# Optimization experiments

Hardware: AMD Instinct MI355X
Metric: run time of the kernel (lower is better)

Reference implementation:

```python
import jax, jax.numpy as jnp
import numpy as np

B, IMG, D, HEADS, L, PC, PF, OUT = 8, 128, 128, 4, 2, 8, 4, 32
HC = IMG // PC; NC = HC * HC          # 16x16 -> 256 coarse tokens
HF = IMG // PF; NF = HF * HF          # 32x32 -> 1024 fine tokens


def _ln(x, g, b):
    m = x.mean(-1, keepdims=True)
    v = x.var(-1, keepdims=True)
    return (x - m) * jax.lax.rsqrt(v + 1e-5) * g + b


def _conv(x, w, b, pad):
    y = jax.lax.conv_general_dilated(x, w, (1, 1), ((pad, pad), (pad, pad)),
                                     dimension_numbers=('NCHW', 'OIHW', 'NCHW'))
    return y + b[None, :, None, None]


def _bilinear_ac(x, oh, ow):  # F.interpolate(mode='bilinear', align_corners=True)
    _, _, H, W = x.shape
    ys = jnp.linspace(0.0, H - 1.0, oh)
    xs = jnp.linspace(0.0, W - 1.0, ow)
    y0 = jnp.floor(ys).astype(jnp.int32); y1 = jnp.minimum(y0 + 1, H - 1); wy = (ys - y0)[:, None]
    x0 = jnp.floor(xs).astype(jnp.int32); x1 = jnp.minimum(x0 + 1, W - 1); wx = (xs - x0)[None, :]
    g = lambda yi, xi: x[:, :, yi][:, :, :, xi]
    return (g(y0, x0) * (1 - wy) * (1 - wx) + g(y0, x1) * (1 - wy) * wx
            + g(y1, x0) * wy * (1 - wx) + g(y1, x1) * wy * wx)


def _patchify(x, p):  # F.unfold with kernel=stride=p, in_chans=1
    b, _, h, w = x.shape
    return x.reshape(b, h // p, p, w // p, p).transpose(0, 1, 3, 2, 4).reshape(b, (h // p) * (w // p), p * p)


def _forward(x, Wpc, bpc, Wpf, bpf, type_embed, ln1_g, ln1_b, Wqkv, Wo, bo,
             ln2_g, ln2_b, W1, b1, W2, b2, dWc, dbc, dWf, dbf, fW1, fb1, fW2, fb2):
    Bx = x.shape[0]
    # ---- multi-scale patch embed ----
    coarse = _patchify(x, PC) @ Wpc + bpc + type_embed[0]   # [B,NC,D]
    fine = _patchify(x, PF) @ Wpf + bpf                     # [B,NF,D]
    # ---- edge map: sobel -> avgpool(4) -> threshold at per-image mean ----
    gray = x.mean(1, keepdims=True)
    kx = jnp.array([[[[-1, 0, 1], [-2, 0, 2], [-1, 0, 1]]]], x.dtype)
    ky = jnp.array([[[[-1, -2, -1], [0, 0, 0], [1, 2, 1]]]], x.dtype)
    sx = _conv(gray, kx, jnp.zeros((1,), x.dtype), 1)
    sy = _conv(gray, ky, jnp.zeros((1,), x.dtype), 1)
    e = jnp.sqrt(sx ** 2 + sy ** 2)
    e = e.reshape(Bx, 1, IMG // 4, 4, IMG // 4, 4).mean((3, 5))  # [B,1,32,32] == fine grid
    mask_flat = (e > e.mean((2, 3), keepdims=True)).reshape(Bx, NF)
    # ---- static-shape analogue of per-sample masked gather + pad_sequence:
    # stable sort puts edge tokens first (original pixel order preserved), pads are zeros
    order = jnp.argsort(jnp.logical_not(mask_flat), axis=1, stable=True)   # [B,NF]
    mask_sorted = jnp.take_along_axis(mask_flat, order, 1)
    fine_sorted = jnp.take_along_axis(fine, order[..., None], 1) * mask_sorted[..., None]
    fine_sorted = fine_sorted + type_embed[1]   # type embed added to pads too (as in torch)
    tokens = jnp.concatenate([coarse, fine_sorted], axis=1)   # [B,N,D]
    N = NC + NF
    hd = D // HEADS
    scale = hd ** -0.5
    # ---- encoder blocks (pre-LN attn + MLP, irregular-token path) ----
    for l in range(L):
        y = _ln(tokens, ln1_g[l], ln1_b[l])
        qkv = (y @ Wqkv[l]).reshape(Bx, N, 3, HEADS, hd).transpose(2, 0, 3, 1, 4)
        q, k, v = qkv[0], qkv[1], qkv[2]
        attn = jax.nn.softmax(jnp.einsum('bhqd,bhkd->bhqk', q, k) * scale, axis=-1)
        o = jnp.einsum('bhqk,bhkd->bhqd', attn, v).transpose(0, 2, 1, 3).reshape(Bx, N, D)
        tokens = tokens + o @ Wo[l] + bo[l]
        y = _ln(tokens, ln2_g[l], ln2_b[l])
        tokens = tokens + jax.nn.gelu(y @ W1[l] + b1[l], approximate=False) @ W2[l] + b2[l]
    # ---- multi-scale decoder ----
    c = (tokens[:, :NC] @ dWc + dbc).reshape(Bx, HC, HC, 1).transpose(0, 3, 1, 2)
    c_up = _bilinear_ac(c, OUT, OUT)
    feats = (tokens[:, NC:] @ dWf + dbf) * mask_sorted[..., None]   # pads stay zero
    inv = jnp.argsort(order, axis=1)                                # scatter back to pixel order
    f_flat = jnp.take_along_axis(feats, inv[..., None], 1)          # [B,NF,1]
    f_map = f_flat.reshape(Bx, HF, HF, 1).transpose(0, 3, 1, 2)
    f_up = _bilinear_ac(f_map, OUT, OUT)
    fused = jnp.concatenate([c_up, f_up], axis=1)
    h = jax.nn.relu(_conv(fused, fW1, fb1, 1))
    return _conv(h, fW2, fb2, 1)   # [B,1,32,32]


def setup_inputs() -> dict:
    key = jax.random.key(0)
    ks = jax.random.split(key, 16)
    n = lambda k, shape: jax.random.normal(k, shape, jnp.float32) * 0.02
    z = lambda *shape: jnp.zeros(shape, jnp.float32)
    return {
        'x': jax.random.normal(ks[0], (B, 1, IMG, IMG), jnp.float32),
        'Wpc': n(ks[1], (PC * PC, D)), 'bpc': z(D),
        'Wpf': n(ks[2], (PF * PF, D)), 'bpf': z(D),
        'type_embed': n(ks[3], (2, D)),
        'ln1_g': jnp.ones((L, D), jnp.float32), 'ln1_b': z(L, D),
        'Wqkv': n(ks[4], (L, D, 3 * D)),
        'Wo': n(ks[5], (L, D, D)), 'bo': z(L, D),
        'ln2_g': jnp.ones((L, D), jnp.float32), 'ln2_b': z(L, D),
        'W1': n(ks[6], (L, D, 2 * D)), 'b1': z(L, 2 * D),
        'W2': n(ks[7], (L, 2 * D, D)), 'b2': z(L, D),
        'dWc': n(ks[8], (D, 1)), 'dbc': z(1),
        'dWf': n(ks[9], (D, 1)), 'dbf': z(1),
        'fW1': n(ks[10], (2, 2, 3, 3)) * 10.0, 'fb1': z(2),
        'fW2': n(ks[11], (1, 2, 3, 3)) * 10.0, 'fb2': z(1),
    }


def reference(x, Wpc, bpc, Wpf, bpf, type_embed, ln1_g, ln1_b, Wqkv, Wo, bo,
              ln2_g, ln2_b, W1, b1, W2, b2, dWc, dbc, dWf, dbf, fW1, fb1, fW2, fb2):
    return _forward(x, Wpc, bpc, Wpf, bpf, type_embed, ln1_g, ln1_b, Wqkv, Wo, bo,
                    ln2_g, ln2_b, W1, b1, W2, b2, dWc, dbc, dWf, dbf, fW1, fb1, fW2, fb2)
```

## Files before the change

### kernel.cpp

```cpp
#include <hip/hip_runtime.h>
#include <math.h>

#define Bx 8
#define IMG 128
#define DD 128
#define HEADS 4
#define LL 2
#define PCc 8
#define PFf 4
#define HCc 16
#define NCc 256
#define HFf 32
#define NFf 1024
#define NTOK 1280
#define HD 32
#define SPLIT 4
#define NQT 20

typedef __attribute__((ext_vector_type(8))) short short8;
typedef __attribute__((ext_vector_type(4))) float f32x4;

__device__ __forceinline__ short f2bf(float f) {
  unsigned u = __builtin_bit_cast(unsigned, f);
  u += 0x7FFF + ((u >> 16) & 1);
  return (short)(u >> 16);
}
__device__ __forceinline__ float bf2f(short s) {
  unsigned u = ((unsigned)(unsigned short)s) << 16;
  return __builtin_bit_cast(float, u);
}

__global__ __launch_bounds__(256) void k_prologue(const float* __restrict__ x,
    const float* __restrict__ Wpc, const float* __restrict__ bpc,
    const float* __restrict__ Wpf, const float* __restrict__ bpf,
    const float* __restrict__ te,
    const float* __restrict__ Wqkv, const float* __restrict__ Wo,
    const float* __restrict__ W1, const float* __restrict__ W2,
    short* __restrict__ WtQKV, short* __restrict__ WtO,
    short* __restrict__ Wt1, short* __restrict__ Wt2,
    float* __restrict__ e, float* __restrict__ tokens,
    float* __restrict__ fineb) {
  int blk = blockIdx.x;
  int t = threadIdx.x;
  if (blk < 1024) {
    int idx = blk * 256 + t;
    int l = idx / 131072, r = idx % 131072;
    const float* src; short* dst; int N, off;
    if (r < 49152)      { src = Wqkv + l * 49152; dst = WtQKV + l * 49152; N = 384; off = r; }
    else if (r < 65536) { src = Wo + l * 16384;  dst = WtO + l * 16384;  N = 128; off = r - 49152; }
    else if (r < 98304) { src = W1 + l * 32768;  dst = Wt1 + l * 32768;  N = 256; off = r - 65536; }
    else                { src = W2 + l * 32768;  dst = Wt2 + l * 32768;  N = 128; off = r - 98304; }
    int k = off / N, n = off % N;
    int K = (r >= 98304) ? 256 : 128;
    dst[(size_t)n * K + k] = f2bf(src[off]);
  } else if (blk < 1536) {
    int bt = blk - 1024;
    int b = bt >> 6, tile = bt & 63;
    int ty = tile >> 3, tx = tile & 7;
    int ly = t >> 4, lx = t & 15;
    int py = ty * 16 + ly, px = tx * 16 + lx;
    const float* img = x + (size_t)b * IMG * IMG;
    float v[3][3];
    #pragma unroll
    for (int ky = 0; ky < 3; ++ky)
      #pragma unroll
      for (int kx = 0; kx < 3; ++kx) {
        int yy = py + ky - 1, xx = px + kx - 1;
        v[ky][kx] = (yy >= 0 && yy < IMG && xx >= 0 && xx < IMG)
                        ? img[yy * IMG + xx] : 0.f;
      }
    float gx = -v[0][0] + v[0][2] - 2.f * v[1][0] + 2.f * v[1][2] - v[2][0] + v[2][2];
    float gy = -v[0][0] - 2.f * v[0][1] - v[0][2] + v[2][0] + 2.f * v[2][1] + v[2][2];
    __shared__ float sm[256];
    sm[t] = sqrtf(gx * gx + gy * gy);
    __syncthreads();
    if (t < 16) {
      int cy = t >> 2, cx = t & 3;
      float s = 0.f;
      #pragma unroll
      for (int dy = 0; dy < 4; ++dy)
        #pragma unroll
        for (int dx = 0; dx < 4; ++dx) s += sm[(cy * 4 + dy) * 16 + cx * 4 + dx];
      e[b * NFf + (ty * 4 + cy) * 32 + tx * 4 + cx] = s * (1.f / 16.f);
    }
  } else if (blk < 2560) {
    int bt = (blk - 1536) * 2 + (t >> 7);
    int b = bt / NCc, tok = bt % NCc;
    int hc = tok / HCc, wc = tok % HCc;
    int half = t >> 7, d = t & 127;
    __shared__ float patch[2][PCc * PCc];
    if (d < PCc * PCc) {
      int pi = d / PCc, pj = d % PCc;
      patch[half][d] = x[(b * IMG + hc * PCc + pi) * IMG + wc * PCc + pj];
    }
    __syncthreads();
    float acc = bpc[d] + te[d];
    #pragma unroll 8
    for (int i = 0; i < PCc * PCc; ++i) acc += patch[half][i] * Wpc[i * DD + d];
    tokens[(size_t)(b * NTOK + tok) * DD + d] = acc;
  } else {
    int ft = (blk - 2560) * 2 + (t >> 7);
    int b = ft >> 10, tloc = ft & 1023;
    int hf = tloc >> 5, wf = tloc & 31;
    int half = t >> 7, d = t & 127;
    __shared__ float patch[2][PFf * PFf];
    if (d < PFf * PFf) {
      int pi = d / PFf, pj = d % PFf;
      patch[half][d] = x[(b * IMG + hf * PFf + pi) * IMG + wf * PFf + pj];
    }
    __syncthreads();
    float acc = bpf[d];
    #pragma unroll
    for (int i = 0; i < PFf * PFf; ++i) acc += patch[half][i] * Wpf[i * DD + d];
    fineb[(size_t)(b * NFf + tloc) * DD + d] = acc;
  }
}

__global__ __launch_bounds__(1024) void k_edge_sort(const float* __restrict__ e,
    int* __restrict__ order, float* __restrict__ msort) {
  int b = blockIdx.x;
  int t = threadIdx.x;
  int lane = t & 63, wave = t >> 6;
  float ev = e[b * NFf + t];
  __shared__ float wsum[16];
  __shared__ int wcnt[16];
  float r = ev;
  #pragma unroll
  for (int o = 32; o > 0; o >>= 1) r += __shfl_xor(r, o, 64);
  if (lane == 0) wsum[wave] = r;
  __syncthreads();
  float tot = 0.f;
  #pragma unroll
  for (int i = 0; i < 16; ++i) tot += wsum[i];
  float mean = tot * (1.f / 1024.f);
  int m = (ev > mean) ? 1 : 0;
  unsigned long long bal = __ballot(m);
  if (lane == 0) wcnt[wave] = __popcll(bal);
  __syncthreads();
  int wbase = 0, total = 0;
  #pragma unroll
  for (int i = 0; i < 16; ++i) {
    int c = wcnt[i];
    if (i < wave) wbase += c;
    total += c;
  }
  unsigned long long below = (lane == 63) ? ~0ULL : ((1ULL << (lane + 1)) - 1);
  int incl = __popcll(bal & below);
  int eb = wbase + incl - m;
  int pos = m ? eb : (total + t - eb);
  order[b * NFf + pos] = t;
  msort[b * NFf + pos] = (float)m;
}

__global__ __launch_bounds__(256) void k_gather_ln(float* __restrict__ tokens,
    const float* __restrict__ fineb, const int* __restrict__ order,
    const float* __restrict__ msort, const float* __restrict__ te,
    const float* __restrict__ g, const float* __restrict__ bb,
    short* __restrict__ outp) {
  int row = blockIdx.x * 4 + (threadIdx.x >> 6);
  int lane = threadIdx.x & 63;
  int b = row / NTOK, r = row % NTOK;
  float2 v;
  if (r < NCc) {
    v = ((const float2*)(tokens + (size_t)row * DD))[lane];
  } else {
    int pos = r - NCc;
    int src = order[b * NFf + pos];
    float mk = msort[b * NFf + pos];
    float2 u = ((const float2*)(fineb + (size_t)(b * NFf + src) * DD))[lane];
    float2 tv = ((const float2*)(te + DD))[lane];
    v.x = u.x * mk + tv.x;
    v.y = u.y * mk + tv.y;
    ((float2*)(tokens + (size_t)row * DD))[lane] = v;
  }
  float s = v.x + v.y;
  #pragma unroll
  for (int o = 32; o > 0; o >>= 1) s += __shfl_xor(s, o, 64);
  float mean = s * (1.f / 128.f);
  float cx = v.x - mean, cy = v.y - mean;
  float q = cx * cx + cy * cy;
  #pragma unroll
  for (int o = 32; o > 0; o >>= 1) q += __shfl_xor(q, o, 64);
  float rstd = rsqrtf(q * (1.f / 128.f) + 1e-5f);
  float2 gg = ((const float2*)g)[lane];
  float2 bv = ((const float2*)bb)[lane];
  int p = (int)(unsigned short)f2bf(cx * rstd * gg.x + bv.x)
        | ((int)(unsigned short)f2bf(cy * rstd * gg.y + bv.y) << 16);
  ((int*)(outp + (size_t)row * DD))[lane] = p;
}

__global__ __launch_bounds__(256) void k_gemm_mfma(const short* __restrict__ A,
    const short* __restrict__ Wt, const float* __restrict__ bias,
    float* __restrict__ Cf, short* __restrict__ Cb, int K, int N, int do_gelu) {
  __shared__ short Alds[64 * 128];
  __shared__ short Blds[64 * 128];
  int row0 = blockIdx.x * 64, col0 = blockIdx.y * 64;
  int t = threadIdx.x;
  int lane = t & 63, w = t >> 6;
  int m = lane & 15, quad = lane >> 4;
  int lrow = lane >> 4, jphys = lane & 15;
  f32x4 zero = {0.f, 0.f, 0.f, 0.f};
  f32x4 acc[4] = {zero, zero, zero, zero};

  for (int kb = 0; kb < K; kb += 128) {
    __syncthreads();
    #pragma unroll
    for (int j = 0; j < 4; ++j) {
      int c = j * 4 + w;
      int r = c * 4 + lrow;
      int jlog = jphys ^ (r & 15);
      __builtin_amdgcn_global_load_lds(
          (const unsigned*)&A[(size_t)(row0 + r) * K + kb + jlog * 8],
          (unsigned*)&Alds[c * 512], 16, 0, 0);
      __builtin_amdgcn_global_load_lds(
          (const unsigned*)&Wt[(size_t)(col0 + r) * K + kb + jlog * 8],
          (unsigned*)&Blds[c * 512], 16, 0, 0);
    }
    __syncthreads();
    #pragma unroll
    for (int ks = 0; ks < 4; ++ks) {
      int pc = ((quad + ks * 4) ^ m) * 8;
      short8 af = *(const short8*)&Alds[(w * 16 + m) * 128 + pc];
      #pragma unroll
      for (int nt = 0; nt < 4; ++nt) {
        short8 bf = *(const short8*)&Blds[(nt * 16 + m) * 128 + pc];
        acc[nt] = __builtin_amdgcn_mfma_f32_16x16x32_bf16(af, bf, acc[nt], 0, 0, 0);
      }
    }
  }
  #pragma unroll
  for (int nt = 0; nt < 4; ++nt) {
    int col = col0 + nt * 16 + m;
    float bv = bias ? bias[col] : 0.f;
    #pragma unroll
    for (int r = 0; r < 4; ++r) {
      int row = row0 + w * 16 + quad * 4 + r;
      float v = acc[nt][r] + bv;
      if (do_gelu) v = 0.5f * v * (1.f + erff(v * 0.70710678118654752f));
      if (Cf) Cf[(size_t)row * N + col] += v;
      else    Cb[(size_t)row * N + col] = f2bf(v);
    }
  }
}

__global__ __launch_bounds__(256) void k_gemm_wo_ln(const short* __restrict__ Opart,
    const float* __restrict__ Lpart, const short* __restrict__ Wt,
    const float* __restrict__ bias, float* __restrict__ tokens,
    const float* __restrict__ lng, const float* __restrict__ lnb,
    short* __restrict__ ybuf) {
  __shared__ short Alds[32 * 136];
  __shared__ short Blds[128 * 128];
  __shared__ float pls[2][32], plq[2][32];
  int row0 = blockIdx.x * 32;
  int b = row0 / NTOK;
  int rloc = row0 % NTOK;
  int qt = rloc >> 6, qoff = rloc & 63;
  int t = threadIdx.x;
  int lane = t & 63, w = t >> 6;
  int m = lane & 15, quad = lane >> 4;
  int rt = w >> 1, ch = w & 1;
  int lrow = lane >> 4, jphys = lane & 15;
  f32x4 zero = {0.f, 0.f, 0.f, 0.f};
  f32x4 acc[4] = {zero, zero, zero, zero};

  #pragma unroll
  for (int j = 0; j < 8; ++j) {
    int c = j * 4 + w;
    int r = c * 4 + lrow;
    int jlog = jphys ^ (r & 15);
    __builtin_amdgcn_global_load_lds(
        (const unsigned*)&Wt[(size_t)r * 128 + jlog * 8],
        (unsigned*)&Blds[c * 512], 16, 0, 0);
  }
  #pragma unroll
  for (int it = 0; it < 2; ++it) {
    int idx = t + it * 256;
    int q = idx >> 4, j = idx & 15;
    int hh = j >> 2, dd = (j & 3) * 8;
    int qg = qoff + q;
    size_t pb = ((size_t)(b * HEADS + hh) * NQT + qt) * SPLIT;
    float L = Lpart[(pb + 0) * 64 + qg] + Lpart[(pb + 1) * 64 + qg]
            + Lpart[(pb + 2) * 64 + qg] + Lpart[(pb + 3) * 64 + qg];
    float o[8] = {0, 0, 0, 0, 0, 0, 0, 0};
    #pragma unroll
    for (int sk = 0; sk < SPLIT; ++sk) {
      short8 po = *(const short8*)&Opart[(pb + sk) * 2048 + qg * 32 + dd];
      #pragma unroll
      for (int i = 0; i < 8; ++i) o[i] += bf2f(po[i]);
    }
    float rs = 1.f / L;
    short8 ov;
    #pragma unroll
    for (int i = 0; i < 8; ++i) ov[i] = f2bf(o[i] * rs);
    *(short8*)&Alds[q * 136 + j * 8] = ov;
  }
  __syncthreads();
  #pragma unroll
  for (int ks = 0; ks < 4; ++ks) {
    short8 af = *(const short8*)&Alds[(rt * 16 + m) * 136 + quad * 8 + ks * 32];
    int pc = ((quad + ks * 4) ^ m) * 8;
    #pragma unroll
    for (int nt = 0; nt < 4; ++nt) {
      short8 bf = *(const short8*)&Blds[(ch * 64 + nt * 16 + m) * 128 + pc];
      acc[nt] = __builtin_amdgcn_mfma_f32_16x16x32_bf16(af, bf, acc[nt], 0, 0, 0);
    }
  }
  float v[4][4];
  #pragma unroll
  for (int nt = 0; nt < 4; ++nt) {
    int col = ch * 64 + nt * 16 + m;
    float bv = bias[col];
    #pragma unroll
    for (int r = 0; r < 4; ++r) {
      int row = row0 + rt * 16 + quad * 4 + r;
      float val = acc[nt][r] + bv + tokens[(size_t)row * DD + col];
      tokens[(size_t)row * DD + col] = val;
      v[nt][r] = val;
    }
  }
  #pragma unroll
  for (int r = 0; r < 4; ++r) {
    float s = v[0][r] + v[1][r] + v[2][r] + v[3][r];
    float q = v[0][r] * v[0][r] + v[1][r] * v[1][r]
            + v[2][r] * v[2][r] + v[3][r] * v[3][r];
    #pragma unroll
    for (int o = 1; o < 16; o <<= 1) { s += __shfl_xor(s, o); q += __shfl_xor(q, o); }
    if (m == 0) {
      int lr = rt * 16 + quad * 4 + r;
      pls[ch][lr] = s;
      plq[ch][lr] = q;
    }
  }
  __syncthreads();
  #pragma unroll
  for (int r = 0; r < 4; ++r) {
    int lr = rt * 16 + quad * 4 + r;
    float S = pls[0][lr] + pls[1][lr];
    float Q = plq[0][lr] + plq[1][lr];
    float mean = S * (1.f / 128.f);
    float var = Q * (1.f / 128.f) - mean * mean;
    float rstd = rsqrtf(var + 1e-5f);
    int row = row0 + lr;
    #pragma unroll
    for (int nt = 0; nt < 4; ++nt) {
      int col = ch * 64 + nt * 16 + m;
      ybuf[(size_t)row * DD + col] = f2bf((v[nt][r] - mean) * rstd * lng[col] + lnb[col]);
    }
  }
}

__global__ __launch_bounds__(256) void k_gemm_mlp(const short* __restrict__ A,
    const short* __restrict__ Wt1, const float* __restrict__ b1,
    const short* __restrict__ Wt2, const float* __restrict__ b2,
    float* __restrict__ tokens, const float* __restrict__ lng,
    const float* __restrict__ lnb, short* __restrict__ ybuf) {
  __shared__ short Alds[32 * 128];
  __shared__ short Blds[128 * 128];
  __shared__ short Hlds[32 * 268];
  __shared__ float pls[2][32], plq[2][32];
  int row0 = blockIdx.x * 32;
  int t = threadIdx.x;
  int lane = t & 63, w = t >> 6;
  int m = lane & 15, quad = lane >> 4;
  int rt = w >> 1, ch = w & 1;
  int lrow = lane >> 4, jphys = lane & 15;
  f32x4 zero = {0.f, 0.f, 0.f, 0.f};

  #pragma unroll
  for (int j = 0; j < 2; ++j) {
    int c = j * 4 + w;
    int r = c * 4 + lrow;
    int jlog = jphys ^ (r & 15);
    __builtin_amdgcn_global_load_lds(
        (const unsigned*)&A[(size_t)(row0 + r) * 128 + jlog * 8],
        (unsigned*)&Alds[c * 512], 16, 0, 0);
  }
  for (int hh = 0; hh < 2; ++hh) {
    #pragma unroll
    for (int j = 0; j < 8; ++j) {
      int c = j * 4 + w;
      int r = c * 4 + lrow;
      int jlog = jphys ^ (r & 15);
      __builtin_amdgcn_global_load_lds(
          (const unsigned*)&Wt1[(size_t)(hh * 128 + r) * 128 + jlog * 8],
          (unsigned*)&Blds[c * 512], 16, 0, 0);
    }
    __syncthreads();
    f32x4 acc[4] = {zero, zero, zero, zero};
    #pragma unroll
    for (int ks = 0; ks < 4; ++ks) {
      int pc = ((quad + ks * 4) ^ m) * 8;
      short8 af = *(const short8*)&Alds[(rt * 16 + m) * 128 + pc];
      #pragma unroll
      for (int nt = 0; nt < 4; ++nt) {
        short8 bf = *(const short8*)&Blds[(ch * 64 + nt * 16 + m) * 128 + pc];
        acc[nt] = __builtin_amdgcn_mfma_f32_16x16x32_bf16(af, bf, acc[nt], 0, 0, 0);
      }
    }
    #pragma unroll
    for (int nt = 0; nt < 4; ++nt) {
      int n = hh * 128 + ch * 64 + nt * 16 + m;
      float bv = b1[n];
      #pragma unroll
      for (int r = 0; r < 4; ++r) {
        float v = acc[nt][r] + bv;
        v = 0.5f * v * (1.f + erff(v * 0.70710678118654752f));
        Hlds[(rt * 16 + quad * 4 + r) * 268 + n] = f2bf(v);
      }
    }
    __syncthreads();
  }
  f32x4 acc[4] = {zero, zero, zero, zero};
  for (int kb = 0; kb < 2; ++kb) {
    if (kb) __syncthreads();
    #pragma unroll
    for (int j = 0; j < 8; ++j) {
      int c = j * 4 + w;
      int r = c * 4 + lrow;
      int jlog = jphys ^ (r & 15);
      __builtin_amdgcn_global_load_lds(
          (const unsigned*)&Wt2[(size_t)r * 256 + kb * 128 + jlog * 8],
          (unsigned*)&Blds[c * 512], 16, 0, 0);
    }
    __syncthreads();
    #pragma unroll
    for (int ks = 0; ks < 4; ++ks) {
      int pc = ((quad + ks * 4) ^ m) * 8;
      short8 af = *(const short8*)&Hlds[(rt * 16 + m) * 268 + kb * 128
                                        + quad * 8 + ks * 32];
      #pragma unroll
      for (int nt = 0; nt < 4; ++nt) {
        short8 bf = *(const short8*)&Blds[(ch * 64 + nt * 16 + m) * 128 + pc];
        acc[nt] = __builtin_amdgcn_mfma_f32_16x16x32_bf16(af, bf, acc[nt], 0, 0, 0);
      }
    }
  }
  float v[4][4];
  #pragma unroll
  for (int nt = 0; nt < 4; ++nt) {
    int col = ch * 64 + nt * 16 + m;
    float bv = b2[col];
    #pragma unroll
    for (int r = 0; r < 4; ++r) {
      int row = row0 + rt * 16 + quad * 4 + r;
      float val = acc[nt][r] + bv + tokens[(size_t)row * DD + col];
      tokens[(size_t)row * DD + col] = val;
      v[nt][r] = val;
    }
  }
  if (ybuf) {
    #pragma unroll
    for (int r = 0; r < 4; ++r) {
      float s = v[0][r] + v[1][r] + v[2][r] + v[3][r];
      float q = v[0][r] * v[0][r] + v[1][r] * v[1][r]
              + v[2][r] * v[2][r] + v[3][r] * v[3][r];
      #pragma unroll
      for (int o = 1; o < 16; o <<= 1) { s += __shfl_xor(s, o); q += __shfl_xor(q, o); }
      if (m == 0) {
        int lr = rt * 16 + quad * 4 + r;
        pls[ch][lr] = s;
        plq[ch][lr] = q;
      }
    }
    __syncthreads();
    #pragma unroll
    for (int r = 0; r < 4; ++r) {
      int lr = rt * 16 + quad * 4 + r;
      float S = pls[0][lr] + pls[1][lr];
      float Q = plq[0][lr] + plq[1][lr];
      float mean = S * (1.f / 128.f);
      float var = Q * (1.f / 128.f) - mean * mean;
      float rstd = rsqrtf(var + 1e-5f);
      int row = row0 + lr;
      #pragma unroll
      for (int nt = 0; nt < 4; ++nt) {
        int col = ch * 64 + nt * 16 + m;
        ybuf[(size_t)row * DD + col] = f2bf((v[nt][r] - mean) * rstd * lng[col] + lnb[col]);
      }
    }
  }
}

__global__ __launch_bounds__(256) void k_attn4(const short* __restrict__ qkv,
    short* __restrict__ Opart, float* __restrict__ Lpart) {
  __shared__ short Ks[64 * 32];
  __shared__ short Vt[32 * 74];
  __shared__ short Pl[4][16 * 74];

  int sk = blockIdx.x % SPLIT;
  int qt = (blockIdx.x / SPLIT) % NQT;
  int h  = (blockIdx.x / (SPLIT * NQT)) % HEADS;
  int b  = blockIdx.x / (SPLIT * NQT * HEADS);
  int t = threadIdx.x;
  int lane = t & 63, w = t >> 6;
  int m = lane & 15, quad = lane >> 4;
  int q0 = qt * 64 + w * 16;

  const float scale = 0.17677669529663687f;
  short8 qraw = *(const short8*)(qkv + ((size_t)(b * NTOK) + q0 + m) * 384 + h * HD + quad * 8);
  short8 qf;
  #pragma unroll
  for (int j = 0; j < 8; ++j) qf[j] = f2bf(bf2f(qraw[j]) * scale);

  f32x4 zero = {0.f, 0.f, 0.f, 0.f};
  f32x4 Oacc[2] = {zero, zero};
  float psum[4] = {0.f, 0.f, 0.f, 0.f};

  int skey = t >> 2, sdseg = t & 3;
  int jlogK = sdseg ^ ((skey >> 1) & 3);
  const short* kstage = qkv + ((size_t)(b * NTOK) + skey) * 384 + 128 + h * HD + jlogK * 8;
  const short* vstage = qkv + ((size_t)(b * NTOK) + skey) * 384 + 256 + h * HD + sdseg * 8;
  int kswz = (quad ^ ((m >> 1) & 3)) * 8;

  for (int s = sk * 5; s < sk * 5 + 5; ++s) {
    __syncthreads();
    __builtin_amdgcn_global_load_lds((const unsigned*)(kstage + (size_t)s * 64 * 384),
                                     (unsigned*)&Ks[w * 512], 16, 0, 0);
    short8 vf = *(const short8*)(vstage + (size_t)s * 64 * 384);
    #pragma unroll
    for (int j = 0; j < 8; ++j) Vt[(sdseg * 8 + j) * 74 + skey] = vf[j];
    __syncthreads();

    f32x4 sc[4];
    #pragma unroll
    for (int ct = 0; ct < 4; ++ct) {
      short8 kfrag = *(const short8*)&Ks[(ct * 16 + m) * 32 + kswz];
      sc[ct] = __builtin_amdgcn_mfma_f32_16x16x32_bf16(qf, kfrag, zero, 0, 0, 0);
    }
    #pragma unroll
    for (int ct = 0; ct < 4; ++ct)
      #pragma unroll
      for (int r = 0; r < 4; ++r) {
        float p = __expf(sc[ct][r]);
        unsigned u = __builtin_bit_cast(unsigned, p);
        psum[r] += __builtin_bit_cast(float, u & 0xffff0000u);
        Pl[w][(quad * 4 + r) * 74 + ct * 16 + m] = (short)(u >> 16);
      }
    #pragma unroll
    for (int ks = 0; ks < 2; ++ks) {
      short8 pfrag = *(const short8*)&Pl[w][m * 74 + ks * 32 + quad * 8];
      #pragma unroll
      for (int nt = 0; nt < 2; ++nt) {
        short8 vfrag = *(const short8*)&Vt[(nt * 16 + m) * 74 + ks * 32 + quad * 8];
        Oacc[nt] = __builtin_amdgcn_mfma_f32_16x16x32_bf16(pfrag, vfrag, Oacc[nt], 0, 0, 0);
      }
    }
  }
  #pragma unroll
  for (int r = 0; r < 4; ++r) {
    float ssum = psum[r];
    #pragma unroll
    for (int o = 1; o < 16; o <<= 1) ssum += __shfl_xor(ssum, o);
    int qloc = w * 16 + quad * 4 + r;
    #pragma unroll
    for (int nt = 0; nt < 2; ++nt)
      Opart[(size_t)blockIdx.x * 2048 + qloc * 32 + nt * 16 + m] = f2bf(Oacc[nt][r]);
    if (m == 0) Lpart[(size_t)blockIdx.x * 64 + qloc] = ssum;
  }
}

__global__ __launch_bounds__(1024) void k_decoder(const float* __restrict__ tokens,
    const float* __restrict__ dWc, const float* __restrict__ dbc,
    const float* __restrict__ dWf, const float* __restrict__ dbf,
    const float* __restrict__ msort, const int* __restrict__ order,
    const float* __restrict__ fW1, const float* __restrict__ fb1,
    const float* __restrict__ fW2, const float* __restrict__ fb2,
    float* __restrict__ outp) {
  int b = blockIdx.x;
  int t = threadIdx.x;
  __shared__ float cmap[NCc];
  __shared__ float fmap[1024];
  __shared__ float cup[1024];
  __shared__ float hb[2][1024];
  {
    const float* row = tokens + (size_t)(b * NTOK + NCc + t) * DD;
    float a = 0.f;
    #pragma unroll 8
    for (int d4 = 0; d4 < 32; ++d4) {
      float4 u = ((const float4*)row)[d4];
      float4 wv = ((const float4*)dWf)[d4];
      a += u.x * wv.x + u.y * wv.y + u.z * wv.z + u.w * wv.w;
    }
    a = (a + dbf[0]) * msort[b * NFf + t];
    fmap[order[b * NFf + t]] = a;
  }
  if (t < NCc) {
    const float* row = tokens + (size_t)(b * NTOK + t) * DD;
    float a = 0.f;
    #pragma unroll 8
    for (int d4 = 0; d4 < 32; ++d4) {
      float4 u = ((const float4*)row)[d4];
      float4 wv = ((const float4*)dWc)[d4];
      a += u.x * wv.x + u.y * wv.y + u.z * wv.z + u.w * wv.w;
    }
    cmap[t] = a + dbc[0];
  }
  __syncthreads();
  int y = t >> 5, x = t & 31;
  {
    float ys = y * (15.f / 31.f);
    float xs = x * (15.f / 31.f);
    int y0 = (int)floorf(ys); int y1 = min(y0 + 1, 15); float wy = ys - (float)y0;
    int x0 = (int)floorf(xs); int x1 = min(x0 + 1, 15); float wx = xs - (float)x0;
    cup[t] = cmap[y0 * 16 + x0] * (1.f - wy) * (1.f - wx)
           + cmap[y0 * 16 + x1] * (1.f - wy) * wx
           + cmap[y1 * 16 + x0] * wy * (1.f - wx)
           + cmap[y1 * 16 + x1] * wy * wx;
  }
  __syncthreads();
  for (int oc = 0; oc < 2; ++oc) {
    float a = fb1[oc];
    #pragma unroll
    for (int ic = 0; ic < 2; ++ic)
      #pragma unroll
      for (int ky = 0; ky < 3; ++ky)
        #pragma unroll
        for (int kx = 0; kx < 3; ++kx) {
          int yy = y + ky - 1, xx = x + kx - 1;
          float v = 0.f;
          if (yy >= 0 && yy < 32 && xx >= 0 && xx < 32)
            v = ic == 0 ? cup[yy * 32 + xx] : fmap[yy * 32 + xx];
          a += v * fW1[((oc * 2 + ic) * 3 + ky) * 3 + kx];
        }
    hb[oc][t] = fmaxf(a, 0.f);
  }
  __syncthreads();
  float a = fb2[0];
  #pragma unroll
  for (int ic = 0; ic < 2; ++ic)
    #pragma unroll
    for (int ky = 0; ky < 3; ++ky)
      #pragma unroll
      for (int kx = 0; kx < 3; ++kx) {
        int yy = y + ky - 1, xx = x + kx - 1;
        float v = (yy >= 0 && yy < 32 && xx >= 0 && xx < 32)
                      ? hb[ic][yy * 32 + xx] : 0.f;
        a += v * fW2[(ic * 3 + ky) * 3 + kx];
      }
  outp[b * 1024 + t] = a;
}

extern "C" void kernel_launch(void* const* d_in, const int* in_sizes, int n_in,
                              void* d_out, int out_size, void* d_ws, size_t ws_size,
                              hipStream_t stream) {
  const float* x    = (const float*)d_in[0];
  const float* Wpc  = (const float*)d_in[1];
  const float* bpc  = (const float*)d_in[2];
  const float* Wpf  = (const float*)d_in[3];
  const float* bpf  = (const float*)d_in[4];
  const float* te   = (const float*)d_in[5];
  const float* ln1g = (const float*)d_in[6];
  const float* ln1b = (const float*)d_in[7];
  const float* Wqkv = (const float*)d_in[8];
  const float* Wo   = (const float*)d_in[9];
  const float* bo   = (const float*)d_in[10];
  const float* ln2g = (const float*)d_in[11];
  const float* ln2b = (const float*)d_in[12];
  const float* W1   = (const float*)d_in[13];
  const float* b1   = (const float*)d_in[14];
  const float* W2   = (const float*)d_in[15];
  const float* b2   = (const float*)d_in[16];
  const float* dWc  = (const float*)d_in[17];
  const float* dbc  = (const float*)d_in[18];
  const float* dWf  = (const float*)d_in[19];
  const float* dbf  = (const float*)d_in[20];
  const float* fW1  = (const float*)d_in[21];
  const float* fb1  = (const float*)d_in[22];
  const float* fW2  = (const float*)d_in[23];
  const float* fb2  = (const float*)d_in[24];

  char* ws = (char*)d_ws;
  float* tokens = (float*)ws;                 ws += 1310720 * 4;
  float* fineb  = (float*)ws;                 ws += 1048576 * 4;
  short* ybuf   = (short*)ws;                 ws += 1310720 * 2;
  short* qkvb   = (short*)ws;                 ws += 3932160 * 2;
  short* Opart  = (short*)ws;                 ws += (size_t)(Bx * HEADS * NQT * SPLIT) * 2048 * 2;
  float* Lpart  = (float*)ws;                 ws += (size_t)(Bx * HEADS * NQT * SPLIT) * 64 * 4;
  short* WtQKV  = (short*)ws;                 ws += 98304 * 2;
  short* WtO    = (short*)ws;                 ws += 32768 * 2;
  short* Wt1    = (short*)ws;                 ws += 65536 * 2;
  short* Wt2    = (short*)ws;                 ws += 65536 * 2;
  float* ebuf   = (float*)ws;                 ws += 8192 * 4;
  float* msort  = (float*)ws;                 ws += 8192 * 4;
  int*   order  = (int*)ws;                   ws += 8192 * 4;

  const int M = Bx * NTOK;

  k_prologue<<<6656, 256, 0, stream>>>(x, Wpc, bpc, Wpf, bpf, te, Wqkv, Wo, W1, W2,
                                       WtQKV, WtO, Wt1, Wt2, ebuf, tokens, fineb);
  k_edge_sort<<<Bx, 1024, 0, stream>>>(ebuf, order, msort);
  k_gather_ln<<<M / 4, 256, 0, stream>>>(tokens, fineb, order, msort, te,
                                         ln1g, ln1b, ybuf);

  for (int l = 0; l < LL; ++l) {
    k_gemm_mfma<<<dim3(M / 64, 384 / 64), 256, 0, stream>>>(
        ybuf, WtQKV + (size_t)l * 49152, nullptr, nullptr, qkvb, 128, 384, 0);
    k_attn4<<<Bx * HEADS * NQT * SPLIT, 256, 0, stream>>>(qkvb, Opart, Lpart);
    k_gemm_wo_ln<<<M / 32, 256, 0, stream>>>(
        Opart, Lpart, WtO + (size_t)l * 16384, bo + l * DD, tokens,
        ln2g + l * DD, ln2b + l * DD, ybuf);
    k_gemm_mlp<<<M / 32, 256, 0, stream>>>(
        ybuf, Wt1 + (size_t)l * 32768, b1 + l * 256,
        Wt2 + (size_t)l * 32768, b2 + l * DD, tokens,
        (l == 0) ? (ln1g + DD) : nullptr, (l == 0) ? (ln1b + DD) : nullptr,
        (l == 0) ? ybuf : nullptr);
  }

  k_decoder<<<Bx, 1024, 0, stream>>>(tokens, dWc, dbc, dWf, dbf, msort, order,
                                     fW1, fb1, fW2, fb2, (float*)d_out);
}
```

Measured before the change: 245.6 us.

## Fuse Wo projection, LN2, MLP, LN1 and next-layer QKV GEMM into one kernel

Merges the post-attention output projection with LN2, the full MLP, the next layer's LN1 and its QKV projection into a single kernel per 32-row tile. Intermediates such as the LN outputs, the hidden activations and the residual stay in LDS and registers instead of round-tripping through global memory, and each layer launches fewer kernels. The cost is higher LDS use per block, which may lower occupancy, and a longer serial chain of weight loads inside each block.

```diff
diff --git a/kernel.cpp b/kernel.cpp
--- a/kernel.cpp
+++ b/kernel.cpp
@@ -243,13 +243,17 @@
   }
 }
 
-__global__ __launch_bounds__(256) void k_gemm_wo_ln(const short* __restrict__ Opart,
-    const float* __restrict__ Lpart, const short* __restrict__ Wt,
-    const float* __restrict__ bias, float* __restrict__ tokens,
-    const float* __restrict__ lng, const float* __restrict__ lnb,
-    short* __restrict__ ybuf) {
-  __shared__ short Alds[32 * 136];
+__global__ __launch_bounds__(256) void k_fused(const short* __restrict__ Opart,
+    const float* __restrict__ Lpart, const short* __restrict__ WtO,
+    const float* __restrict__ bo_, const float* __restrict__ ln2g_,
+    const float* __restrict__ ln2b_, const short* __restrict__ Wt1,
+    const float* __restrict__ b1_, const short* __restrict__ Wt2,
+    const float* __restrict__ b2_, float* __restrict__ tokens,
+    const float* __restrict__ ln1g_, const float* __restrict__ ln1b_,
+    const short* __restrict__ WtQ, short* __restrict__ qkvb) {
   __shared__ short Blds[128 * 128];
+  __shared__ short AH[32 * 268];
+  __shared__ short Ylds[32 * 136];
   __shared__ float pls[2][32], plq[2][32];
   int row0 = blockIdx.x * 32;
   int b = row0 / NTOK;
@@ -261,7 +265,6 @@
   int rt = w >> 1, ch = w & 1;
   int lrow = lane >> 4, jphys = lane & 15;
   f32x4 zero = {0.f, 0.f, 0.f, 0.f};
-  f32x4 acc[4] = {zero, zero, zero, zero};
 
   #pragma unroll
   for (int j = 0; j < 8; ++j) {
@@ -269,16 +272,16 @@
     int r = c * 4 + lrow;
     int jlog = jphys ^ (r & 15);
     __builtin_amdgcn_global_load_lds(
-        (const unsigned*)&Wt[(size_t)r * 128 + jlog * 8],
+        (const unsigned*)&WtO[(size_t)r * 128 + jlog * 8],
         (unsigned*)&Blds[c * 512], 16, 0, 0);
   }
   #pragma unroll
   for (int it = 0; it < 2; ++it) {
     int idx = t + it * 256;
     int q = idx >> 4, j = idx & 15;
-    int hh = j >> 2, dd = (j & 3) * 8;
+    int dh = j >> 2, dd = (j & 3) * 8;
     int qg = qoff + q;
-    size_t pb = ((size_t)(b * HEADS + hh) * NQT + qt) * SPLIT;
+    size_t pb = ((size_t)(b * HEADS + dh) * NQT + qt) * SPLIT;
     float L = Lpart[(pb + 0) * 64 + qg] + Lpart[(pb + 1) * 64 + qg]
             + Lpart[(pb + 2) * 64 + qg] + Lpart[(pb + 3) * 64 + qg];
     float o[8] = {0, 0, 0, 0, 0, 0, 0, 0};
@@ -292,12 +295,13 @@
     short8 ov;
     #pragma unroll
     for (int i = 0; i < 8; ++i) ov[i] = f2bf(o[i] * rs);
-    *(short8*)&Alds[q * 136 + j * 8] = ov;
+    *(short8*)&AH[q * 136 + j * 8] = ov;
   }
   __syncthreads();
+  f32x4 acc[4] = {zero, zero, zero, zero};
   #pragma unroll
   for (int ks = 0; ks < 4; ++ks) {
-    short8 af = *(const short8*)&Alds[(rt * 16 + m) * 136 + quad * 8 + ks * 32];
+    short8 af = *(const short8*)&AH[(rt * 16 + m) * 136 + quad * 8 + ks * 32];
     int pc = ((quad + ks * 4) ^ m) * 8;
     #pragma unroll
     for (int nt = 0; nt < 4; ++nt) {
@@ -309,13 +313,11 @@
   #pragma unroll
   for (int nt = 0; nt < 4; ++nt) {
     int col = ch * 64 + nt * 16 + m;
-    float bv = bias[col];
+    float bv = bo_[col];
     #pragma unroll
     for (int r = 0; r < 4; ++r) {
       int row = row0 + rt * 16 + quad * 4 + r;
-      float val = acc[nt][r] + bv + tokens[(size_t)row * DD + col];
-      tokens[(size_t)row * DD + col] = val;
-      v[nt][r] = val;
+      v[nt][r] = acc[nt][r] + bv + tokens[(size_t)row * DD + col];
     }
   }
   #pragma unroll
@@ -340,40 +342,11 @@
     float mean = S * (1.f / 128.f);
     float var = Q * (1.f / 128.f) - mean * mean;
     float rstd = rsqrtf(var + 1e-5f);
-    int row = row0 + lr;
     #pragma unroll
     for (int nt = 0; nt < 4; ++nt) {
       int col = ch * 64 + nt * 16 + m;
-      ybuf[(size_t)row * DD + col] = f2bf((v[nt][r] - mean) * rstd * lng[col] + lnb[col]);
-    }
-  }
-}
-
-__global__ __launch_bounds__(256) void k_gemm_mlp(const short* __restrict__ A,
-    const short* __restrict__ Wt1, const float* __restrict__ b1,
-    const short* __restrict__ Wt2, const float* __restrict__ b2,
-    float* __restrict__ tokens, const float* __restrict__ lng,
-    const float* __restrict__ lnb, short* __restrict__ ybuf) {
-  __shared__ short Alds[32 * 128];
-  __shared__ short Blds[128 * 128];
-  __shared__ short Hlds[32 * 268];
-  __shared__ float pls[2][32], plq[2][32];
-  int row0 = blockIdx.x * 32;
-  int t = threadIdx.x;
-  int lane = t & 63, w = t >> 6;
-  int m = lane & 15, quad = lane >> 4;
-  int rt = w >> 1, ch = w & 1;
-  int lrow = lane >> 4, jphys = lane & 15;
-  f32x4 zero = {0.f, 0.f, 0.f, 0.f};
-
-  #pragma unroll
-  for (int j = 0; j < 2; ++j) {
-    int c = j * 4 + w;
-    int r = c * 4 + lrow;
-    int jlog = jphys ^ (r & 15);
-    __builtin_amdgcn_global_load_lds(
-        (const unsigned*)&A[(size_t)(row0 + r) * 128 + jlog * 8],
-        (unsigned*)&Alds[c * 512], 16, 0, 0);
+      Ylds[lr * 136 + col] = f2bf((v[nt][r] - mean) * rstd * ln2g_[col] + ln2b_[col]);
+    }
   }
   for (int hh = 0; hh < 2; ++hh) {
     #pragma unroll
@@ -386,31 +359,31 @@
           (unsigned*)&Blds[c * 512], 16, 0, 0);
     }
     __syncthreads();
-    f32x4 acc[4] = {zero, zero, zero, zero};
+    f32x4 ha[4] = {zero, zero, zero, zero};
     #pragma unroll
     for (int ks = 0; ks < 4; ++ks) {
+      short8 af = *(const short8*)&Ylds[(rt * 16 + m) * 136 + quad * 8 + ks * 32];
       int pc = ((quad + ks * 4) ^ m) * 8;
-      short8 af = *(const short8*)&Alds[(rt * 16 + m) * 128 + pc];
       #pragma unroll
       for (int nt = 0; nt < 4; ++nt) {
         short8 bf = *(const short8*)&Blds[(ch * 64 + nt * 16 + m) * 128 + pc];
-        acc[nt] = __builtin_amdgcn_mfma_f32_16x16x32_bf16(af, bf, acc[nt], 0, 0, 0);
+        ha[nt] = __builtin_amdgcn_mfma_f32_16x16x32_bf16(af, bf, ha[nt], 0, 0, 0);
       }
     }
     #pragma unroll
     for (int nt = 0; nt < 4; ++nt) {
       int n = hh * 128 + ch * 64 + nt * 16 + m;
-      float bv = b1[n];
+      float bv = b1_[n];
       #pragma unroll
       for (int r = 0; r < 4; ++r) {
-        float v = acc[nt][r] + bv;
-        v = 0.5f * v * (1.f + erff(v * 0.70710678118654752f));
-        Hlds[(rt * 16 + quad * 4 + r) * 268 + n] = f2bf(v);
-      }
-    }
-    __syncthreads();
-  }
-  f32x4 acc[4] = {zero, zero, zero, zero};
+        float vv = ha[nt][r] + bv;
+        vv = 0.5f * vv * (1.f + erff(vv * 0.70710678118654752f));
+        AH[(rt * 16 + quad * 4 + r) * 268 + n] = f2bf(vv);
+      }
+    }
+    __syncthreads();
+  }
+  f32x4 a2[4] = {zero, zero, zero, zero};
   for (int kb = 0; kb < 2; ++kb) {
     if (kb) __syncthreads();
     #pragma unroll
@@ -426,56 +399,86 @@
     #pragma unroll
     for (int ks = 0; ks < 4; ++ks) {
       int pc = ((quad + ks * 4) ^ m) * 8;
-      short8 af = *(const short8*)&Hlds[(rt * 16 + m) * 268 + kb * 128
-                                        + quad * 8 + ks * 32];
+      short8 af = *(const short8*)&AH[(rt * 16 + m) * 268 + kb * 128
+                                      + quad * 8 + ks * 32];
       #pragma unroll
       for (int nt = 0; nt < 4; ++nt) {
         short8 bf = *(const short8*)&Blds[(ch * 64 + nt * 16 + m) * 128 + pc];
-        acc[nt] = __builtin_amdgcn_mfma_f32_16x16x32_bf16(af, bf, acc[nt], 0, 0, 0);
-      }
-    }
-  }
-  float v[4][4];
+        a2[nt] = __builtin_amdgcn_mfma_f32_16x16x32_bf16(af, bf, a2[nt], 0, 0, 0);
+      }
+    }
+  }
   #pragma unroll
   for (int nt = 0; nt < 4; ++nt) {
     int col = ch * 64 + nt * 16 + m;
-    float bv = b2[col];
+    float bv = b2_[col];
     #pragma unroll
     for (int r = 0; r < 4; ++r) {
       int row = row0 + rt * 16 + quad * 4 + r;
-      float val = acc[nt][r] + bv + tokens[(size_t)row * DD + col];
+      float val = a2[nt][r] + bv + v[nt][r];
       tokens[(size_t)row * DD + col] = val;
       v[nt][r] = val;
     }
   }
-  if (ybuf) {
-    #pragma unroll
-    for (int r = 0; r < 4; ++r) {
-      float s = v[0][r] + v[1][r] + v[2][r] + v[3][r];
-      float q = v[0][r] * v[0][r] + v[1][r] * v[1][r]
-              + v[2][r] * v[2][r] + v[3][r] * v[3][r];
-      #pragma unroll
-      for (int o = 1; o < 16; o <<= 1) { s += __shfl_xor(s, o); q += __shfl_xor(q, o); }
-      if (m == 0) {
-        int lr = rt * 16 + quad * 4 + r;
-        pls[ch][lr] = s;
-        plq[ch][lr] = q;
-      }
-    }
-    __syncthreads();
-    #pragma unroll
-    for (int r = 0; r < 4; ++r) {
+  if (ln1g_ == nullptr) return;
+  #pragma unroll
+  for (int r = 0; r < 4; ++r) {
+    float s = v[0][r] + v[1][r] + v[2][r] + v[3][r];
+    float q = v[0][r] * v[0][r] + v[1][r] * v[1][r]
+            + v[2][r] * v[2][r] + v[3][r] * v[3][r];
+    #pragma unroll
+    for (int o = 1; o < 16; o <<= 1) { s += __shfl_xor(s, o); q += __shfl_xor(q, o); }
+    if (m == 0) {
       int lr = rt * 16 + quad * 4 + r;
-      float S = pls[0][lr] + pls[1][lr];
-      float Q = plq[0][lr] + plq[1][lr];
-      float mean = S * (1.f / 128.f);
-      float var = Q * (1.f / 128.f) - mean * mean;
-      float rstd = rsqrtf(var + 1e-5f);
-      int row = row0 + lr;
+      pls[ch][lr] = s;
+      plq[ch][lr] = q;
+    }
+  }
+  __syncthreads();
+  #pragma unroll
+  for (int r = 0; r < 4; ++r) {
+    int lr = rt * 16 + quad * 4 + r;
+    float S = pls[0][lr] + pls[1][lr];
+    float Q = plq[0][lr] + plq[1][lr];
+    float mean = S * (1.f / 128.f);
+    float var = Q * (1.f / 128.f) - mean * mean;
+    float rstd = rsqrtf(var + 1e-5f);
+    #pragma unroll
+    for (int nt = 0; nt < 4; ++nt) {
+      int col = ch * 64 + nt * 16 + m;
+      Ylds[lr * 136 + col] = f2bf((v[nt][r] - mean) * rstd * ln1g_[col] + ln1b_[col]);
+    }
+  }
+  for (int c3 = 0; c3 < 3; ++c3) {
+    if (c3) __syncthreads();
+    #pragma unroll
+    for (int j = 0; j < 8; ++j) {
+      int c = j * 4 + w;
+      int r = c * 4 + lrow;
+      int jlog = jphys ^ (r & 15);
+      __builtin_amdgcn_global_load_lds(
+          (const unsigned*)&WtQ[(size_t)(c3 * 128 + r) * 128 + jlog * 8],
+          (unsigned*)&Blds[c * 512], 16, 0, 0);
+    }
+    __syncthreads();
+    f32x4 qa[4] = {zero, zero, zero, zero};
+    #pragma unroll
+    for (int ks = 0; ks < 4; ++ks) {
+      short8 af = *(const short8*)&Ylds[(rt * 16 + m) * 136 + quad * 8 + ks * 32];
+      int pc = ((quad + ks * 4) ^ m) * 8;
       #pragma unroll
       for (int nt = 0; nt < 4; ++nt) {
-        int col = ch * 64 + nt * 16 + m;
-        ybuf[(size_t)row * DD + col] = f2bf((v[nt][r] - mean) * rstd * lng[col] + lnb[col]);
+        short8 bf = *(const short8*)&Blds[(ch * 64 + nt * 16 + m) * 128 + pc];
+        qa[nt] = __builtin_amdgcn_mfma_f32_16x16x32_bf16(af, bf, qa[nt], 0, 0, 0);
+      }
+    }
+    #pragma unroll
+    for (int nt = 0; nt < 4; ++nt) {
+      int col = c3 * 128 + ch * 64 + nt * 16 + m;
+      #pragma unroll
+      for (int r = 0; r < 4; ++r) {
+        int row = row0 + rt * 16 + quad * 4 + r;
+        qkvb[(size_t)row * 384 + col] = f2bf(qa[nt][r]);
       }
     }
   }
@@ -692,19 +695,19 @@
   k_gather_ln<<<M / 4, 256, 0, stream>>>(tokens, fineb, order, msort, te,
                                          ln1g, ln1b, ybuf);
 
-  for (int l = 0; l < LL; ++l) {
-    k_gemm_mfma<<<dim3(M / 64, 384 / 64), 256, 0, stream>>>(
-        ybuf, WtQKV + (size_t)l * 49152, nullptr, nullptr, qkvb, 128, 384, 0);
-    k_attn4<<<Bx * HEADS * NQT * SPLIT, 256, 0, stream>>>(qkvb, Opart, Lpart);
-    k_gemm_wo_ln<<<M / 32, 256, 0, stream>>>(
-        Opart, Lpart, WtO + (size_t)l * 16384, bo + l * DD, tokens,
-        ln2g + l * DD, ln2b + l * DD, ybuf);
-    k_gemm_mlp<<<M / 32, 256, 0, stream>>>(
-        ybuf, Wt1 + (size_t)l * 32768, b1 + l * 256,
-        Wt2 + (size_t)l * 32768, b2 + l * DD, tokens,
-        (l == 0) ? (ln1g + DD) : nullptr, (l == 0) ? (ln1b + DD) : nullptr,
-        (l == 0) ? ybuf : nullptr);
-  }
+  k_gemm_mfma<<<dim3(M / 64, 384 / 64), 256, 0, stream>>>(
+      ybuf, WtQKV, nullptr, nullptr, qkvb, 128, 384, 0);
+  k_attn4<<<Bx * HEADS * NQT * SPLIT, 256, 0, stream>>>(qkvb, Opart, Lpart);
+  k_fused<<<M / 32, 256, 0, stream>>>(
+      Opart, Lpart, WtO, bo, ln2g, ln2b,
+      Wt1, b1, Wt2, b2, tokens,
+      ln1g + DD, ln1b + DD, WtQKV + 49152, qkvb);
+
+  k_attn4<<<Bx * HEADS * NQT * SPLIT, 256, 0, stream>>>(qkvb, Opart, Lpart);
+  k_fused<<<M / 32, 256, 0, stream>>>(
+      Opart, Lpart, WtO + 16384, bo + DD, ln2g + DD, ln2b + DD,
+      Wt1 + 32768, b1 + 256, Wt2 + 32768, b2 + DD, tokens,
+      nullptr, nullptr, nullptr, nullptr);
 
   k_decoder<<<Bx, 1024, 0, stream>>>(tokens, dWc, dbc, dWf, dbf, msort, order,
                                      fW1, fb1, fW2, fb2, (float*)d_out);
```

New measurement: 236.1 us. 3.9% less time.
